# Performance work log

Hardware: AMD Instinct MI355X
Metric: run time of the kernel (lower is better)

The kernel has to match this reference:

```python
import jax, jax.numpy as jnp
import numpy as np
from jax import lax

# Dims matching init_kwargs
T, BK, OBS = 2048, 64, 64   # obs_dim = percept_dim(63) + reward_dim(1)
H, P, N = 16, 64, 64        # nheads, headdim, d_state; d_inner = H*P = 1024
DIN = H * P


def setup_inputs() -> dict:
    key = jax.random.key(0)
    ks = jax.random.split(key, 12)
    s = lambda fan_in: 1.0 / np.sqrt(fan_in)
    return {
        "obs": jax.random.normal(ks[0], (T, BK, OBS), jnp.float32),
        "reward": jax.random.normal(ks[1], (T, BK, 1), jnp.float32),
        "W_in": jax.random.normal(ks[2], (OBS, DIN), jnp.float32) * s(OBS),
        "W_B": jax.random.normal(ks[3], (OBS, N), jnp.float32) * s(OBS),
        "W_C": jax.random.normal(ks[4], (OBS, N), jnp.float32) * s(OBS),
        "W_dt": jax.random.normal(ks[5], (1, H), jnp.float32),
        "dt_bias": jax.random.normal(ks[6], (H,), jnp.float32) * 0.5,
        "A_log": jax.random.uniform(ks[7], (H,), jnp.float32, 0.0, 1.0),
        "D": jax.random.normal(ks[8], (H,), jnp.float32),
        "W_out": jax.random.normal(ks[9], (DIN, 1), jnp.float32) * s(DIN),
        "init_state": jax.random.normal(ks[10], (H, P, N), jnp.float32) * 0.1,
        "k": 8,
    }


def reference(obs, reward, W_in, W_B, W_C, W_dt, dt_bias, A_log, D, W_out, init_state, k):
    # obs: (T, Bk, obs_dim), reward: (T, Bk, 1)
    Tn, Bk, _ = obs.shape
    # Precompute per-step projections (vectorized over time)
    u = (obs @ W_in).reshape(Tn, Bk, H, P)      # (T,Bk,H,P) input stream
    Bm = obs @ W_B                              # (T,Bk,N) input-dependent B
    Cm = obs @ W_C                              # (T,Bk,N) input-dependent C
    dt = jax.nn.softplus(reward @ W_dt + dt_bias)  # (T,Bk,H) reward-modulated dt
    A = -jnp.exp(A_log)                          # (H,) negative decay rates
    decay = jnp.exp(dt * A)                     # (T,Bk,H)

    # Cache init: zeros + initial_states (per QAgent.forward)
    h0 = jnp.broadcast_to(init_state, (Bk, H, P, N))

    def step(h, inp):
        u_t, B_t, C_t, dt_t, dec_t = inp
        # selective-scan state update: h = h*exp(dt*A) + dt*u (outer) B
        h = h * dec_t[..., None, None] + (dt_t[..., None] * u_t)[..., None] * B_t[:, None, None, :]
        y = jnp.einsum('bhpn,bn->bhp', h, C_t) + D[None, :, None] * u_t
        o = y.reshape(Bk, DIN) @ W_out          # (Bk, 1) scalar Q per option
        return h, o

    _, ys = lax.scan(step, h0, (u, Bm, Cm, dt, decay))  # ys: (T, Bk, 1)
    q = ys.reshape(Tn, -1, k)                   # (T, B, k)
    logits = q
    return q, logits
```

## Files before the change

### kernel.cpp

```cpp
#include <hip/hip_runtime.h>
#include <math.h>

#define TT     2048
#define BKK    64
#define OBSD   64
#define NH     16
#define PDIM   64
#define NSTATE 64
#define DINN   1024
#define TB     (TT*BKK)
#define NC     32
#define CL     (TT/NC)

#define RS      164
#define OFF_C   64
#define OFF_DEC 128
#define OFF_XW  144
#define OFF_OB  160

template <int CTRL>
__device__ __forceinline__ float dpp_add(float x) {
    int y = __builtin_amdgcn_update_dpp(0, __float_as_int(x), CTRL, 0xF, 0xF, true);
    return x + __int_as_float(y);
}
__device__ __forceinline__ float wave_sum_lane63(float x) {
    x = dpp_add<0x111>(x);
    x = dpp_add<0x112>(x);
    x = dpp_add<0x114>(x);
    x = dpp_add<0x118>(x);
    x = dpp_add<0x142>(x);
    x = dpp_add<0x143>(x);
    return x;
}

__device__ __forceinline__ float softplusf(float z) {
    return (z > 20.f) ? z : log1pf(expf(z));
}

__global__ void dup_q(float* __restrict__ q) {
    int i = blockIdx.x * 256 + threadIdx.x;
    if (i < TB) q[TB + i] = q[i];
}

__global__ __launch_bounds__(1024)
void init_proj(const float* __restrict__ Win, const float* __restrict__ Wout,
               const float* __restrict__ initS,
               float* __restrict__ wproj, float* __restrict__ g0) {
    const int tid = threadIdx.x;
    {
        const int k = tid >> 4, h = tid & 15;
        float s = 0.f;
#pragma unroll 8
        for (int p = 0; p < PDIM; ++p)
            s = fmaf(Win[(size_t)k * DINN + h * 64 + p], Wout[h * 64 + p], s);
        wproj[tid] = s;
    }
    {
        const int h = tid >> 6, n = tid & 63;
        float s = 0.f;
#pragma unroll 8
        for (int p = 0; p < PDIM; ++p)
            s = fmaf(initS[h * PDIM * NSTATE + p * NSTATE + n], Wout[h * 64 + p], s);
        g0[tid] = s;
    }
}

__global__ __launch_bounds__(256)
void prelude2(const float* __restrict__ obs, const float* __restrict__ reward,
              const float* __restrict__ WB, const float* __restrict__ WC,
              const float* __restrict__ Wdt, const float* __restrict__ dtb,
              const float* __restrict__ Alog, const float* __restrict__ Dv,
              const float* __restrict__ wproj, float* __restrict__ rows) {
    int gw = (blockIdx.x * 256 + threadIdx.x) >> 6;
    gw = __builtin_amdgcn_readfirstlane(gw);
    const int lane = threadIdx.x & 63;
    const int row0 = gw * 8;
    if (row0 >= TB) return;

    const int h = lane & 15;
    const int q = lane >> 4;

    const float wdt_h = Wdt[h];
    const float dtb_h = dtb[h];
    const float A_h   = -expf(Alog[h]);
    const float D_h   = Dv[h];
    float wpj[16];
#pragma unroll
    for (int j = 0; j < 16; ++j)
        wpj[j] = wproj[(q * 16 + j) * 16 + h];

    float aB[8], aC[8];
#pragma unroll
    for (int r = 0; r < 8; ++r) { aB[r] = 0.f; aC[r] = 0.f; }
#pragma unroll 8
    for (int kk = 0; kk < OBSD; ++kk) {
        float wb = WB[kk * 64 + lane];
        float wc = WC[kk * 64 + lane];
#pragma unroll
        for (int r = 0; r < 8; ++r) {
            float o = obs[(size_t)(row0 + r) * OBSD + kk];
            aB[r] = fmaf(o, wb, aB[r]);
            aC[r] = fmaf(o, wc, aC[r]);
        }
    }

#pragma unroll 1
    for (int r = 0; r < 8; ++r) {
        const int row = row0 + r;
        float* rb = rows + (size_t)row * RS;
        rb[lane]         = aB[r];
        rb[OFF_C + lane] = aC[r];

        const float4* oq = (const float4*)(obs + (size_t)row * OBSD + q * 16);
        float4 o0 = oq[0], o1 = oq[1], o2 = oq[2], o3 = oq[3];
        float wpart = 0.f;
        wpart = fmaf(o0.x, wpj[0],  wpart); wpart = fmaf(o0.y, wpj[1],  wpart);
        wpart = fmaf(o0.z, wpj[2],  wpart); wpart = fmaf(o0.w, wpj[3],  wpart);
        wpart = fmaf(o1.x, wpj[4],  wpart); wpart = fmaf(o1.y, wpj[5],  wpart);
        wpart = fmaf(o1.z, wpj[6],  wpart); wpart = fmaf(o1.w, wpj[7],  wpart);
        wpart = fmaf(o2.x, wpj[8],  wpart); wpart = fmaf(o2.y, wpj[9],  wpart);
        wpart = fmaf(o2.z, wpj[10], wpart); wpart = fmaf(o2.w, wpj[11], wpart);
        wpart = fmaf(o3.x, wpj[12], wpart); wpart = fmaf(o3.y, wpj[13], wpart);
        wpart = fmaf(o3.z, wpj[14], wpart); wpart = fmaf(o3.w, wpj[15], wpart);
        wpart += __shfl_xor(wpart, 16, 64);
        wpart += __shfl_xor(wpart, 32, 64);

        const float rew  = reward[row];
        const float dtv  = softplusf(fmaf(rew, wdt_h, dtb_h));
        const float decv = expf(dtv * A_h);
        const float xwv  = dtv * wpart;
        if (q == 0) rb[OFF_DEC + h] = decv;
        if (q == 1) rb[OFF_XW  + h] = xwv;

        float dw = D_h * wpart;
        dw += __shfl_xor(dw, 1, 64);
        dw += __shfl_xor(dw, 2, 64);
        dw += __shfl_xor(dw, 4, 64);
        dw += __shfl_xor(dw, 8, 64);
        if (lane == 0) rb[OFF_OB] = dw;
    }
}

__global__ __launch_bounds__(256)
void phaseA(const float* __restrict__ rows, float* __restrict__ Send,
            float* __restrict__ Ptot) {
    int w = (blockIdx.x * 256 + threadIdx.x) >> 6;
    w = __builtin_amdgcn_readfirstlane(w);
    const int lane = threadIdx.x & 63;
    const int b = w & 63;
    const int c = w >> 6;

    const float* rowp = rows + ((size_t)(c * CL) * BKK + b) * RS;
    float g[16], Pc[16];
#pragma unroll
    for (int hh = 0; hh < 16; ++hh) { g[hh] = 0.f; Pc[hh] = 1.f; }

    float Bv = rowp[lane];

#pragma unroll 2
    for (int i = 0; i < CL; ++i) {
        const float* nxt = rowp + (size_t)RS * BKK;
        float Bn = 0.f;
        if (i < CL - 1) Bn = nxt[lane];
#pragma unroll
        for (int hh = 0; hh < 16; ++hh) {
            const float dh = rowp[OFF_DEC + hh];
            g[hh] = fmaf(g[hh], dh, rowp[OFF_XW + hh] * Bv);
            Pc[hh] *= dh;
        }
        rowp = nxt; Bv = Bn;
    }

    const size_t base = ((size_t)c * BKK + b) * 16;
#pragma unroll
    for (int hh = 0; hh < 16; ++hh)
        Send[(base + hh) * 64 + lane] = g[hh];
    if (lane == 0) {
#pragma unroll
        for (int hh = 0; hh < 16; ++hh)
            Ptot[base + hh] = Pc[hh];
    }
}

__global__ __launch_bounds__(64)
void phaseB(const float* __restrict__ g0, const float* __restrict__ Send,
            const float* __restrict__ Ptot, float* __restrict__ gcbuf) {
    const int b    = blockIdx.x;
    const int lane = threadIdx.x;

    float g[16];
#pragma unroll
    for (int hh = 0; hh < 16; ++hh)
        g[hh] = g0[hh * 64 + lane];

#pragma unroll 1
    for (int c = 0; c < NC; ++c) {
        const size_t base = ((size_t)c * BKK + b) * 16;
#pragma unroll
        for (int hh = 0; hh < 16; ++hh)
            gcbuf[(base + hh) * 64 + lane] = g[hh];
        if (c < NC - 1) {
#pragma unroll
            for (int hh = 0; hh < 16; ++hh)
                g[hh] = fmaf(Ptot[base + hh], g[hh], Send[(base + hh) * 64 + lane]);
        }
    }
}

__global__ __launch_bounds__(256)
void phaseC(const float* __restrict__ rows, const float* __restrict__ gcbuf,
            float* __restrict__ qout) {
    int w = (blockIdx.x * 256 + threadIdx.x) >> 6;
    w = __builtin_amdgcn_readfirstlane(w);
    const int lane = threadIdx.x & 63;
    const int b = w & 63;
    const int c = w >> 6;

    const size_t base = ((size_t)c * BKK + b) * 16;
    float g[16];
#pragma unroll
    for (int hh = 0; hh < 16; ++hh)
        g[hh] = gcbuf[(base + hh) * 64 + lane];

    const float* rowp = rows + ((size_t)(c * CL) * BKK + b) * RS;
    float Bv = rowp[lane];
    float Cv = rowp[OFF_C + lane];

#pragma unroll 2
    for (int i = 0; i < CL; ++i) {
        const float* nxt = rowp + (size_t)RS * BKK;
        float Bn = 0.f, Cn = 0.f;
        if (i < CL - 1) { Bn = nxt[lane]; Cn = nxt[OFF_C + lane]; }

        float y = 0.f;
#pragma unroll
        for (int hh = 0; hh < 16; ++hh) {
            g[hh] = fmaf(g[hh], rowp[OFF_DEC + hh], rowp[OFF_XW + hh] * Bv);
            y = fmaf(g[hh], Cv, y);
        }
        const float ob = rowp[OFF_OB];

        float tot = wave_sum_lane63(y);
        if (lane == 63) qout[(size_t)(c * CL + i) * BKK + b] = tot + ob;

        rowp = nxt; Bv = Bn; Cv = Cn;
    }
}

__global__ __launch_bounds__(64)
void scan3_kernel(const float* __restrict__ rows, const float* __restrict__ g0,
                  float* __restrict__ qout) {
    const int b    = blockIdx.x;
    const int lane = threadIdx.x;

    float g[16];
#pragma unroll
    for (int hh = 0; hh < 16; ++hh)
        g[hh] = g0[hh * 64 + lane];

    const float* rowp = rows + (size_t)b * RS;
    float Bv = rowp[lane];
    float Cv = rowp[OFF_C + lane];

#pragma unroll 2
    for (int t = 0; t < TT; ++t) {
        const float* nrow = rowp + (size_t)RS * BKK;
        float Bn = 0.f, Cn = 0.f;
        if (t < TT - 1) { Bn = nrow[lane]; Cn = nrow[OFF_C + lane]; }

        float y = 0.f;
#pragma unroll
        for (int hh = 0; hh < 16; ++hh) {
            float tmp = rowp[OFF_XW + hh] * Bv;
            g[hh] = fmaf(g[hh], rowp[OFF_DEC + hh], tmp);
            y = fmaf(g[hh], Cv, y);
        }
        const float ob = rowp[OFF_OB];

        float tot = wave_sum_lane63(y);
        if (lane == 63) qout[(size_t)t * BKK + b] = tot + ob;

        rowp = nrow; Bv = Bn; Cv = Cn;
    }
}

extern "C" void kernel_launch(void* const* d_in, const int* in_sizes, int n_in,
                              void* d_out, int out_size, void* d_ws, size_t ws_size,
                              hipStream_t stream) {
    const float* obs    = (const float*)d_in[0];
    const float* reward = (const float*)d_in[1];
    const float* Win    = (const float*)d_in[2];
    const float* WB     = (const float*)d_in[3];
    const float* WC     = (const float*)d_in[4];
    const float* Wdt    = (const float*)d_in[5];
    const float* dtb    = (const float*)d_in[6];
    const float* Alog   = (const float*)d_in[7];
    const float* Dv     = (const float*)d_in[8];
    const float* Wout   = (const float*)d_in[9];
    const float* initS  = (const float*)d_in[10];
    float* qout = (float*)d_out;

    const size_t n_rows = (size_t)TB * RS;
    const size_t n_cs   = (size_t)NC * BKK * 16 * 64;
    const size_t n_pt   = (size_t)NC * BKK * 16;

    const size_t need1 = (n_rows + 2048) * 4;
    const size_t need2 = (n_rows + 2048 + 2 * n_cs + n_pt) * 4;

    float* rows  = (float*)d_ws;
    float* wproj = rows + n_rows;
    float* g0    = wproj + 1024;

    if (ws_size >= need2) {
        float* Send  = g0 + 1024;
        float* gcbuf = Send + n_cs;
        float* Ptot  = gcbuf + n_cs;
        hipLaunchKernelGGL(init_proj, dim3(1),        dim3(1024), 0, stream,
                           Win, Wout, initS, wproj, g0);
        hipLaunchKernelGGL(prelude2,  dim3(TB / 32),  dim3(256),  0, stream,
                           obs, reward, WB, WC, Wdt, dtb, Alog, Dv, wproj, rows);
        hipLaunchKernelGGL(phaseA,    dim3(512),      dim3(256),  0, stream,
                           rows, Send, Ptot);
        hipLaunchKernelGGL(phaseB,    dim3(BKK),      dim3(64),   0, stream,
                           g0, Send, Ptot, gcbuf);
        hipLaunchKernelGGL(phaseC,    dim3(512),      dim3(256),  0, stream,
                           rows, gcbuf, qout);
        hipLaunchKernelGGL(dup_q,     dim3(TB / 256), dim3(256),  0, stream, qout);
    } else {
        hipLaunchKernelGGL(init_proj, dim3(1),        dim3(1024), 0, stream,
                           Win, Wout, initS, wproj, g0);
        hipLaunchKernelGGL(prelude2,  dim3(TB / 32),  dim3(256),  0, stream,
                           obs, reward, WB, WC, Wdt, dtb, Alog, Dv, wproj, rows);
        hipLaunchKernelGGL(scan3_kernel, dim3(BKK),   dim3(64),   0, stream,
                           rows, g0, qout);
        hipLaunchKernelGGL(dup_q,     dim3(TB / 256), dim3(256),  0, stream, qout);
    }
}
```

Baseline: 256.1 us.

## Recompute B/C projections in scan phases instead of materializing wide row buffer

Removes the B and C projection outputs from the prelude's per-row workspace, shrinking each row from 164 to 40 floats. The chunked scan phases A and C now recompute B (and C) from obs with WB/WC held in registers. Also fuses the q duplication into phaseC, splits init_proj across 8 blocks, prefetches the next chunk's carry data in phaseB, and drops the sequential fallback path. The aim is to cut workspace write and read traffic and a launch, at the cost of redundant FMAs and high register pressure (128 weight floats per lane in phaseC).

```diff
diff --git a/kernel.cpp b/kernel.cpp
--- a/kernel.cpp
+++ b/kernel.cpp
@@ -10,13 +10,8 @@
 #define DINN   1024
 #define TB     (TT*BKK)
 #define NC     32
-#define CL     (TT/NC)
-
-#define RS      164
-#define OFF_C   64
-#define OFF_DEC 128
-#define OFF_XW  144
-#define OFF_OB  160
+#define CL     64
+#define DDS    40
 
 template <int CTRL>
 __device__ __forceinline__ float dpp_add(float x) {
@@ -37,40 +32,50 @@
     return (z > 20.f) ? z : log1pf(expf(z));
 }
 
-__global__ void dup_q(float* __restrict__ q) {
-    int i = blockIdx.x * 256 + threadIdx.x;
-    if (i < TB) q[TB + i] = q[i];
-}
-
-__global__ __launch_bounds__(1024)
-void init_proj(const float* __restrict__ Win, const float* __restrict__ Wout,
-               const float* __restrict__ initS,
-               float* __restrict__ wproj, float* __restrict__ g0) {
-    const int tid = threadIdx.x;
-    {
-        const int k = tid >> 4, h = tid & 15;
+#define LOAD_DX(ptr, dd_, xx_)                                            \
+    {                                                                     \
+        const float4* _p = (const float4*)(ptr);                          \
+        float4 a0 = _p[0], a1 = _p[1], a2 = _p[2], a3 = _p[3];            \
+        float4 b0 = _p[4], b1 = _p[5], b2 = _p[6], b3 = _p[7];            \
+        dd_[0]=a0.x; dd_[1]=a0.y; dd_[2]=a0.z; dd_[3]=a0.w;               \
+        dd_[4]=a1.x; dd_[5]=a1.y; dd_[6]=a1.z; dd_[7]=a1.w;               \
+        dd_[8]=a2.x; dd_[9]=a2.y; dd_[10]=a2.z; dd_[11]=a2.w;             \
+        dd_[12]=a3.x; dd_[13]=a3.y; dd_[14]=a3.z; dd_[15]=a3.w;           \
+        xx_[0]=b0.x; xx_[1]=b0.y; xx_[2]=b0.z; xx_[3]=b0.w;               \
+        xx_[4]=b1.x; xx_[5]=b1.y; xx_[6]=b1.z; xx_[7]=b1.w;               \
+        xx_[8]=b2.x; xx_[9]=b2.y; xx_[10]=b2.z; xx_[11]=b2.w;             \
+        xx_[12]=b3.x; xx_[13]=b3.y; xx_[14]=b3.z; xx_[15]=b3.w;           \
+    }
+
+__global__ __launch_bounds__(256)
+void init_proj2(const float* __restrict__ Win, const float* __restrict__ Wout,
+                const float* __restrict__ initS,
+                float* __restrict__ wproj, float* __restrict__ g0) {
+    const int t = threadIdx.x;
+    if (blockIdx.x < 4) {
+        const int idx = blockIdx.x * 256 + t;
+        const int k = idx >> 4, h = idx & 15;
         float s = 0.f;
 #pragma unroll 8
         for (int p = 0; p < PDIM; ++p)
             s = fmaf(Win[(size_t)k * DINN + h * 64 + p], Wout[h * 64 + p], s);
-        wproj[tid] = s;
-    }
-    {
-        const int h = tid >> 6, n = tid & 63;
+        wproj[idx] = s;
+    } else {
+        const int idx = (blockIdx.x - 4) * 256 + t;
+        const int h = idx >> 6, n = idx & 63;
         float s = 0.f;
 #pragma unroll 8
         for (int p = 0; p < PDIM; ++p)
             s = fmaf(initS[h * PDIM * NSTATE + p * NSTATE + n], Wout[h * 64 + p], s);
-        g0[tid] = s;
+        g0[idx] = s;
     }
 }
 
 __global__ __launch_bounds__(256)
-void prelude2(const float* __restrict__ obs, const float* __restrict__ reward,
-              const float* __restrict__ WB, const float* __restrict__ WC,
+void prelude3(const float* __restrict__ obs, const float* __restrict__ reward,
               const float* __restrict__ Wdt, const float* __restrict__ dtb,
               const float* __restrict__ Alog, const float* __restrict__ Dv,
-              const float* __restrict__ wproj, float* __restrict__ rows) {
+              const float* __restrict__ wproj, float* __restrict__ dd) {
     int gw = (blockIdx.x * 256 + threadIdx.x) >> 6;
     gw = __builtin_amdgcn_readfirstlane(gw);
     const int lane = threadIdx.x & 63;
@@ -89,27 +94,9 @@
     for (int j = 0; j < 16; ++j)
         wpj[j] = wproj[(q * 16 + j) * 16 + h];
 
-    float aB[8], aC[8];
-#pragma unroll
-    for (int r = 0; r < 8; ++r) { aB[r] = 0.f; aC[r] = 0.f; }
-#pragma unroll 8
-    for (int kk = 0; kk < OBSD; ++kk) {
-        float wb = WB[kk * 64 + lane];
-        float wc = WC[kk * 64 + lane];
-#pragma unroll
-        for (int r = 0; r < 8; ++r) {
-            float o = obs[(size_t)(row0 + r) * OBSD + kk];
-            aB[r] = fmaf(o, wb, aB[r]);
-            aC[r] = fmaf(o, wc, aC[r]);
-        }
-    }
-
 #pragma unroll 1
     for (int r = 0; r < 8; ++r) {
         const int row = row0 + r;
-        float* rb = rows + (size_t)row * RS;
-        rb[lane]         = aB[r];
-        rb[OFF_C + lane] = aC[r];
 
         const float4* oq = (const float4*)(obs + (size_t)row * OBSD + q * 16);
         float4 o0 = oq[0], o1 = oq[1], o2 = oq[2], o3 = oq[3];
@@ -129,46 +116,63 @@
         const float dtv  = softplusf(fmaf(rew, wdt_h, dtb_h));
         const float decv = expf(dtv * A_h);
         const float xwv  = dtv * wpart;
-        if (q == 0) rb[OFF_DEC + h] = decv;
-        if (q == 1) rb[OFF_XW  + h] = xwv;
+
+        float* dr = dd + (size_t)row * DDS;
+        if (q == 0) dr[h]      = decv;
+        if (q == 1) dr[16 + h] = xwv;
 
         float dw = D_h * wpart;
         dw += __shfl_xor(dw, 1, 64);
         dw += __shfl_xor(dw, 2, 64);
         dw += __shfl_xor(dw, 4, 64);
         dw += __shfl_xor(dw, 8, 64);
-        if (lane == 0) rb[OFF_OB] = dw;
+        if (lane == 0) dr[32] = dw;
     }
 }
 
 __global__ __launch_bounds__(256)
-void phaseA(const float* __restrict__ rows, float* __restrict__ Send,
-            float* __restrict__ Ptot) {
-    int w = (blockIdx.x * 256 + threadIdx.x) >> 6;
+void phaseA(const float* __restrict__ obs, const float* __restrict__ dd,
+            const float* __restrict__ WB,
+            float* __restrict__ Send, float* __restrict__ Ptot) {
+    int w = blockIdx.x * 4 + (threadIdx.x >> 6);
     w = __builtin_amdgcn_readfirstlane(w);
     const int lane = threadIdx.x & 63;
     const int b = w & 63;
     const int c = w >> 6;
 
-    const float* rowp = rows + ((size_t)(c * CL) * BKK + b) * RS;
+    float wb[64];
+#pragma unroll
+    for (int k = 0; k < 64; ++k) wb[k] = WB[k * 64 + lane];
+
     float g[16], Pc[16];
 #pragma unroll
     for (int hh = 0; hh < 16; ++hh) { g[hh] = 0.f; Pc[hh] = 1.f; }
 
-    float Bv = rowp[lane];
-
-#pragma unroll 2
+    const float* orow = obs + ((size_t)(c * CL) * BKK + b) * OBSD;
+    const float* dr   = dd  + ((size_t)(c * CL) * BKK + b) * DDS;
+
+#pragma unroll 1
     for (int i = 0; i < CL; ++i) {
-        const float* nxt = rowp + (size_t)RS * BKK;
-        float Bn = 0.f;
-        if (i < CL - 1) Bn = nxt[lane];
+        float dec_[16], xw_[16];
+        LOAD_DX(dr, dec_, xw_);
+
+        float s0 = 0.f, s1 = 0.f, s2 = 0.f, s3 = 0.f;
+#pragma unroll
+        for (int k = 0; k < 64; k += 4) {
+            s0 = fmaf(orow[k],     wb[k],     s0);
+            s1 = fmaf(orow[k + 1], wb[k + 1], s1);
+            s2 = fmaf(orow[k + 2], wb[k + 2], s2);
+            s3 = fmaf(orow[k + 3], wb[k + 3], s3);
+        }
+        const float Bv = (s0 + s1) + (s2 + s3);
+
 #pragma unroll
         for (int hh = 0; hh < 16; ++hh) {
-            const float dh = rowp[OFF_DEC + hh];
-            g[hh] = fmaf(g[hh], dh, rowp[OFF_XW + hh] * Bv);
-            Pc[hh] *= dh;
-        }
-        rowp = nxt; Bv = Bn;
+            g[hh] = fmaf(g[hh], dec_[hh], xw_[hh] * Bv);
+            Pc[hh] *= dec_[hh];
+        }
+        orow += (size_t)BKK * OBSD;
+        dr   += (size_t)BKK * DDS;
     }
 
     const size_t base = ((size_t)c * BKK + b) * 16;
@@ -193,94 +197,112 @@
     for (int hh = 0; hh < 16; ++hh)
         g[hh] = g0[hh * 64 + lane];
 
+    float S_[16], P_[16];
+    {
+        const size_t base = (size_t)b * 16;
+#pragma unroll
+        for (int hh = 0; hh < 16; ++hh) S_[hh] = Send[(base + hh) * 64 + lane];
+        const float4* pp = (const float4*)(Ptot + base);
+        float4 a0 = pp[0], a1 = pp[1], a2 = pp[2], a3 = pp[3];
+        P_[0]=a0.x; P_[1]=a0.y; P_[2]=a0.z; P_[3]=a0.w;
+        P_[4]=a1.x; P_[5]=a1.y; P_[6]=a1.z; P_[7]=a1.w;
+        P_[8]=a2.x; P_[9]=a2.y; P_[10]=a2.z; P_[11]=a2.w;
+        P_[12]=a3.x; P_[13]=a3.y; P_[14]=a3.z; P_[15]=a3.w;
+    }
+
 #pragma unroll 1
     for (int c = 0; c < NC; ++c) {
         const size_t base = ((size_t)c * BKK + b) * 16;
+        float Sn[16], Pn[16];
+        if (c < NC - 1) {
+            const size_t nb = ((size_t)(c + 1) * BKK + b) * 16;
+#pragma unroll
+            for (int hh = 0; hh < 16; ++hh) Sn[hh] = Send[(nb + hh) * 64 + lane];
+            const float4* pp = (const float4*)(Ptot + nb);
+            float4 a0 = pp[0], a1 = pp[1], a2 = pp[2], a3 = pp[3];
+            Pn[0]=a0.x; Pn[1]=a0.y; Pn[2]=a0.z; Pn[3]=a0.w;
+            Pn[4]=a1.x; Pn[5]=a1.y; Pn[6]=a1.z; Pn[7]=a1.w;
+            Pn[8]=a2.x; Pn[9]=a2.y; Pn[10]=a2.z; Pn[11]=a2.w;
+            Pn[12]=a3.x; Pn[13]=a3.y; Pn[14]=a3.z; Pn[15]=a3.w;
+        }
 #pragma unroll
         for (int hh = 0; hh < 16; ++hh)
             gcbuf[(base + hh) * 64 + lane] = g[hh];
         if (c < NC - 1) {
 #pragma unroll
-            for (int hh = 0; hh < 16; ++hh)
-                g[hh] = fmaf(Ptot[base + hh], g[hh], Send[(base + hh) * 64 + lane]);
+            for (int hh = 0; hh < 16; ++hh) {
+                g[hh] = fmaf(P_[hh], g[hh], S_[hh]);
+                P_[hh] = Pn[hh]; S_[hh] = Sn[hh];
+            }
         }
     }
 }
 
 __global__ __launch_bounds__(256)
-void phaseC(const float* __restrict__ rows, const float* __restrict__ gcbuf,
-            float* __restrict__ qout) {
-    int w = (blockIdx.x * 256 + threadIdx.x) >> 6;
+void phaseC(const float* __restrict__ obs, const float* __restrict__ dd,
+            const float* __restrict__ WB, const float* __restrict__ WC,
+            const float* __restrict__ gcbuf, float* __restrict__ qout) {
+    int w = blockIdx.x * 4 + (threadIdx.x >> 6);
     w = __builtin_amdgcn_readfirstlane(w);
     const int lane = threadIdx.x & 63;
     const int b = w & 63;
     const int c = w >> 6;
 
-    const size_t base = ((size_t)c * BKK + b) * 16;
+    float wb[64], wc[64];
+#pragma unroll
+    for (int k = 0; k < 64; ++k) wb[k] = WB[k * 64 + lane];
+#pragma unroll
+    for (int k = 0; k < 64; ++k) wc[k] = WC[k * 64 + lane];
+
+    const size_t sbase = ((size_t)c * BKK + b) * 16;
     float g[16];
 #pragma unroll
     for (int hh = 0; hh < 16; ++hh)
-        g[hh] = gcbuf[(base + hh) * 64 + lane];
-
-    const float* rowp = rows + ((size_t)(c * CL) * BKK + b) * RS;
-    float Bv = rowp[lane];
-    float Cv = rowp[OFF_C + lane];
-
-#pragma unroll 2
+        g[hh] = gcbuf[(sbase + hh) * 64 + lane];
+
+    const float* orow = obs + ((size_t)(c * CL) * BKK + b) * OBSD;
+    const float* dr   = dd  + ((size_t)(c * CL) * BKK + b) * DDS;
+
+#pragma unroll 1
     for (int i = 0; i < CL; ++i) {
-        const float* nxt = rowp + (size_t)RS * BKK;
-        float Bn = 0.f, Cn = 0.f;
-        if (i < CL - 1) { Bn = nxt[lane]; Cn = nxt[OFF_C + lane]; }
+        float dec_[16], xw_[16];
+        LOAD_DX(dr, dec_, xw_);
+        const float ob = dr[32];
+
+        float s0 = 0.f, s1 = 0.f, s2 = 0.f, s3 = 0.f;
+        float t0 = 0.f, t1 = 0.f, t2 = 0.f, t3 = 0.f;
+#pragma unroll
+        for (int k = 0; k < 64; k += 4) {
+            const float a0 = orow[k], a1 = orow[k + 1], a2 = orow[k + 2], a3 = orow[k + 3];
+            s0 = fmaf(a0, wb[k],     s0);
+            s1 = fmaf(a1, wb[k + 1], s1);
+            s2 = fmaf(a2, wb[k + 2], s2);
+            s3 = fmaf(a3, wb[k + 3], s3);
+            t0 = fmaf(a0, wc[k],     t0);
+            t1 = fmaf(a1, wc[k + 1], t1);
+            t2 = fmaf(a2, wc[k + 2], t2);
+            t3 = fmaf(a3, wc[k + 3], t3);
+        }
+        const float Bv = (s0 + s1) + (s2 + s3);
+        const float Cv = (t0 + t1) + (t2 + t3);
 
         float y = 0.f;
 #pragma unroll
         for (int hh = 0; hh < 16; ++hh) {
-            g[hh] = fmaf(g[hh], rowp[OFF_DEC + hh], rowp[OFF_XW + hh] * Bv);
+            g[hh] = fmaf(g[hh], dec_[hh], xw_[hh] * Bv);
             y = fmaf(g[hh], Cv, y);
         }
-        const float ob = rowp[OFF_OB];
 
         float tot = wave_sum_lane63(y);
-        if (lane == 63) qout[(size_t)(c * CL + i) * BKK + b] = tot + ob;
-
-        rowp = nxt; Bv = Bn; Cv = Cn;
-    }
-}
-
-__global__ __launch_bounds__(64)
-void scan3_kernel(const float* __restrict__ rows, const float* __restrict__ g0,
-                  float* __restrict__ qout) {
-    const int b    = blockIdx.x;
-    const int lane = threadIdx.x;
-
-    float g[16];
-#pragma unroll
-    for (int hh = 0; hh < 16; ++hh)
-        g[hh] = g0[hh * 64 + lane];
-
-    const float* rowp = rows + (size_t)b * RS;
-    float Bv = rowp[lane];
-    float Cv = rowp[OFF_C + lane];
-
-#pragma unroll 2
-    for (int t = 0; t < TT; ++t) {
-        const float* nrow = rowp + (size_t)RS * BKK;
-        float Bn = 0.f, Cn = 0.f;
-        if (t < TT - 1) { Bn = nrow[lane]; Cn = nrow[OFF_C + lane]; }
-
-        float y = 0.f;
-#pragma unroll
-        for (int hh = 0; hh < 16; ++hh) {
-            float tmp = rowp[OFF_XW + hh] * Bv;
-            g[hh] = fmaf(g[hh], rowp[OFF_DEC + hh], tmp);
-            y = fmaf(g[hh], Cv, y);
-        }
-        const float ob = rowp[OFF_OB];
-
-        float tot = wave_sum_lane63(y);
-        if (lane == 63) qout[(size_t)t * BKK + b] = tot + ob;
-
-        rowp = nrow; Bv = Bn; Cv = Cn;
+        if (lane == 63) {
+            const size_t idx = (size_t)(c * CL + i) * BKK + b;
+            const float v = tot + ob;
+            qout[idx]      = v;
+            qout[TB + idx] = v;
+        }
+
+        orow += (size_t)BKK * OBSD;
+        dr   += (size_t)BKK * DDS;
     }
 }
 
@@ -300,39 +322,21 @@
     const float* initS  = (const float*)d_in[10];
     float* qout = (float*)d_out;
 
-    const size_t n_rows = (size_t)TB * RS;
-    const size_t n_cs   = (size_t)NC * BKK * 16 * 64;
-    const size_t n_pt   = (size_t)NC * BKK * 16;
-
-    const size_t need1 = (n_rows + 2048) * 4;
-    const size_t need2 = (n_rows + 2048 + 2 * n_cs + n_pt) * 4;
-
-    float* rows  = (float*)d_ws;
-    float* wproj = rows + n_rows;
+    const size_t n_dd = (size_t)TB * DDS;
+    const size_t n_cs = (size_t)NC * BKK * 16 * 64;
+    const size_t n_pt = (size_t)NC * BKK * 16;
+
+    float* dd    = (float*)d_ws;
+    float* Send  = dd + n_dd;
+    float* gcbuf = Send + n_cs;
+    float* Ptot  = gcbuf + n_cs;
+    float* wproj = Ptot + n_pt;
     float* g0    = wproj + 1024;
 
-    if (ws_size >= need2) {
-        float* Send  = g0 + 1024;
-        float* gcbuf = Send + n_cs;
-        float* Ptot  = gcbuf + n_cs;
-        hipLaunchKernelGGL(init_proj, dim3(1),        dim3(1024), 0, stream,
-                           Win, Wout, initS, wproj, g0);
-        hipLaunchKernelGGL(prelude2,  dim3(TB / 32),  dim3(256),  0, stream,
-                           obs, reward, WB, WC, Wdt, dtb, Alog, Dv, wproj, rows);
-        hipLaunchKernelGGL(phaseA,    dim3(512),      dim3(256),  0, stream,
-                           rows, Send, Ptot);
-        hipLaunchKernelGGL(phaseB,    dim3(BKK),      dim3(64),   0, stream,
-                           g0, Send, Ptot, gcbuf);
-        hipLaunchKernelGGL(phaseC,    dim3(512),      dim3(256),  0, stream,
-                           rows, gcbuf, qout);
-        hipLaunchKernelGGL(dup_q,     dim3(TB / 256), dim3(256),  0, stream, qout);
-    } else {
-        hipLaunchKernelGGL(init_proj, dim3(1),        dim3(1024), 0, stream,
-                           Win, Wout, initS, wproj, g0);
-        hipLaunchKernelGGL(prelude2,  dim3(TB / 32),  dim3(256),  0, stream,
-                           obs, reward, WB, WC, Wdt, dtb, Alog, Dv, wproj, rows);
-        hipLaunchKernelGGL(scan3_kernel, dim3(BKK),   dim3(64),   0, stream,
-                           rows, g0, qout);
-        hipLaunchKernelGGL(dup_q,     dim3(TB / 256), dim3(256),  0, stream, qout);
-    }
-}
+    init_proj2<<<dim3(8), dim3(256), 0, stream>>>(Win, Wout, initS, wproj, g0);
+    prelude3<<<dim3(TB / 32), dim3(256), 0, stream>>>(obs, reward, Wdt, dtb,
+                                                      Alog, Dv, wproj, dd);
+    phaseA<<<dim3(512), dim3(256), 0, stream>>>(obs, dd, WB, Send, Ptot);
+    phaseB<<<dim3(BKK), dim3(64), 0, stream>>>(g0, Send, Ptot, gcbuf);
+    phaseC<<<dim3(512), dim3(256), 0, stream>>>(obs, dd, WB, WC, gcbuf, qout);
+}
```

After: 308.3 us. 20.4% more time.
